# Kernel optimization log

Hardware: AMD Instinct MI355X
Metric: run time of the kernel (lower is better)

Reference implementation:

```python
import jax, jax.numpy as jnp
import numpy as np

EMBED_DIM = 256
H = 80
W = 80
N_HEADS = 8
N_POINTS = 4
B = 8


def sine_pe(C, h, w):
    # LoFTR-style PositionEncodingSine, returns [1, C, h, w]
    y_pos = jnp.cumsum(jnp.ones((h, w), jnp.float32), axis=0)[None]
    x_pos = jnp.cumsum(jnp.ones((h, w), jnp.float32), axis=1)[None]
    div = jnp.exp(jnp.arange(0, C // 2, 2, dtype=jnp.float32) * (-np.log(10000.0) / (C // 2)))[:, None, None]
    pe = jnp.zeros((C, h, w), jnp.float32)
    pe = pe.at[0::4].set(jnp.sin(x_pos * div))
    pe = pe.at[1::4].set(jnp.cos(x_pos * div))
    pe = pe.at[2::4].set(jnp.sin(y_pos * div))
    pe = pe.at[3::4].set(jnp.cos(y_pos * div))
    return pe[None]


def make_reference_points(h, w):
    # Faithful to the original (W-major flatten, (col, row) stacking)
    gr = np.linspace(0, 1, w)
    gc = np.linspace(0, 1, h)
    R, Cg = np.meshgrid(gr, gc, indexing='ij')  # (w, h)
    ref = np.stack((Cg, R), -1).reshape(-1, 2)  # [w*h, 2]
    return jnp.asarray(ref, jnp.float32)


def setup_inputs():
    key = jax.random.key(0)
    ks = jax.random.split(key, 8)
    C = EMBED_DIM
    s = 1.0 / np.sqrt(C)
    return {
        'query': jax.random.normal(ks[0], (B, C, H, W), jnp.float32),
        'value': jax.random.normal(ks[1], (B, C, H, W), jnp.float32),
        'W_value': jax.random.normal(ks[2], (C, C), jnp.float32) * s,
        'b_value': jnp.zeros((C,), jnp.float32),
        'W_off': jax.random.normal(ks[3], (C, N_HEADS * N_POINTS * 2), jnp.float32) * 0.01,
        'b_off': jax.random.normal(ks[4], (N_HEADS * N_POINTS * 2,), jnp.float32) * 0.5,
        'W_attn': jax.random.normal(ks[5], (C, N_HEADS * N_POINTS), jnp.float32) * s,
        'b_attn': jnp.zeros((N_HEADS * N_POINTS,), jnp.float32),
        'W_out': jax.random.normal(ks[6], (C, C), jnp.float32) * s,
        'b_out': jnp.zeros((C,), jnp.float32),
    }


def _deform_attn_core(q, v, ref, W_off, b_off, W_attn, b_attn):
    # q: [B, Nq, C] queries; v: [B, H*W, C] projected values; ref: [Nq, 2]
    Bq, Nq, C = q.shape
    hd = C // N_HEADS
    off = (q @ W_off + b_off).reshape(Bq, Nq, N_HEADS, N_POINTS, 2)
    aw = jax.nn.softmax((q @ W_attn + b_attn).reshape(Bq, Nq, N_HEADS, N_POINTS), axis=-1)
    norm = jnp.array([W, H], jnp.float32)  # offset normalizer (W, H), num_levels=1
    loc = ref[None, :, None, None, :] + off / norm  # [B, Nq, Hn, P, 2], normalized (x, y)
    loc = loc.transpose(0, 2, 1, 3, 4)  # [B, Hn, Nq, P, 2]
    # grid_sample(align_corners=False, padding_mode='zeros'): pixel = loc*size - 0.5
    x = loc[..., 0] * W - 0.5
    y = loc[..., 1] * H - 0.5
    x0f = jnp.floor(x); y0f = jnp.floor(y)
    wx = x - x0f; wy = y - y0f
    x0 = x0f.astype(jnp.int32); y0 = y0f.astype(jnp.int32)
    vh = v.reshape(Bq, H * W, N_HEADS, hd).transpose(0, 2, 1, 3)  # [B, Hn, HW, hd]

    def gather(ix, iy):
        valid = (ix >= 0) & (ix < W) & (iy >= 0) & (iy < H)
        idx = jnp.clip(iy, 0, H - 1) * W + jnp.clip(ix, 0, W - 1)  # [B, Hn, Nq, P]
        g = jnp.take_along_axis(vh, idx.reshape(Bq, N_HEADS, -1, 1), axis=2)
        return g.reshape(Bq, N_HEADS, Nq, N_POINTS, hd) * valid[..., None].astype(v.dtype)

    samp = (gather(x0, y0) * ((1 - wx) * (1 - wy))[..., None]
            + gather(x0 + 1, y0) * (wx * (1 - wy))[..., None]
            + gather(x0, y0 + 1) * ((1 - wx) * wy)[..., None]
            + gather(x0 + 1, y0 + 1) * (wx * wy)[..., None])  # [B, Hn, Nq, P, hd]
    out = jnp.einsum('bhqpd,bhqp->bqhd', samp, aw.transpose(0, 2, 1, 3))
    return out.reshape(Bq, Nq, C)


def reference(query, value, W_value, b_value, W_off, b_off, W_attn, b_attn, W_out, b_out):
    pe = sine_pe(EMBED_DIM, H, W)
    q = query + pe
    qf = q.reshape(B, EMBED_DIM, H * W).transpose(0, 2, 1)      # [B, Nq, C]
    vf = value.reshape(B, EMBED_DIM, H * W).transpose(0, 2, 1)  # [B, Nv, C]
    vproj = vf @ W_value + b_value
    ref = make_reference_points(H, W)
    attn = _deform_attn_core(qf, vproj, ref, W_off, b_off, W_attn, b_attn)
    attn = attn @ W_out + b_out
    attn = attn + qf  # mmcv MSDeformAttn residual (dropout identity at eval)
    out_img = attn.transpose(0, 2, 1).reshape(B, EMBED_DIM, H, W)
    # nn.Upsample(size=(H, W), bilinear) on an (H, W) map is identity (need_downsample=False)
    return (out_img + value, out_img)
```

## Files before the change

### kernel.cpp

```cpp
#include <hip/hip_runtime.h>
#include <hip/hip_bf16.h>
#include <stdint.h>

#define HH 80
#define WW 80
#define NQ 6400
#define CD 256
#define BB 8
#define OUT_HALF 13107200
#define PE_NEG 0.0719557841560639f

typedef __attribute__((ext_vector_type(4))) float f32x4;
typedef __bf16 bf16_t;
typedef __attribute__((ext_vector_type(8))) __bf16 bf16x8;
typedef __attribute__((ext_vector_type(4))) __bf16 bf16x4;
typedef _Float16 f16_t;
typedef __attribute__((ext_vector_type(8))) _Float16 f16x8;

using gp1_t = const __attribute__((address_space(1))) void*;
using lp3_t = __attribute__((address_space(3))) void*;

__device__ __forceinline__ void gload_lds16(const void* g, void* l) {
    __builtin_amdgcn_global_load_lds((gp1_t)g, (lp3_t)l, 16, 0, 0);
}

__global__ __launch_bounds__(256) void pe_kernel(float* __restrict__ pe) {
    int idx = blockIdx.x * 256 + threadIdx.x;
    if (idx >= CD * NQ) return;
    int c = idx / NQ, n = idx % NQ;
    int h = n / WW, w = n % WW;
    int k = c >> 2;
    float d = __expf((float)(2 * k) * -PE_NEG);
    float arg = ((c & 2) ? (float)(h + 1) : (float)(w + 1)) * d;
    float sv, cv;
    __sincosf(arg, &sv, &cv);
    pe[idx] = (c & 1) ? cv : sv;
}

__global__ __launch_bounds__(256) void wprep_kernel(const float* __restrict__ Wv,
                                                    const float* __restrict__ Woff,
                                                    const float* __restrict__ Wattn,
                                                    const float* __restrict__ Wout,
                                                    bf16_t* __restrict__ WvT,
                                                    bf16_t* __restrict__ WoaT,
                                                    bf16_t* __restrict__ WoT) {
    int idx = blockIdx.x * 256 + threadIdx.x;
    if (idx < 65536) {
        int cp = idx >> 8, c = idx & 255;
        WvT[idx] = (bf16_t)Wv[c * 256 + cp];
        WoT[idx] = (bf16_t)Wout[c * 256 + cp];
    }
    if (idx < 96 * 256) {
        int j = idx >> 8, c = idx & 255;
        WoaT[idx] = (bf16_t)(j < 64 ? Woff[c * 64 + j] : Wattn[c * 32 + (j - 64)]);
    }
}


__global__ __launch_bounds__(256, 3) void gemm_vproj(const float* __restrict__ V,
                                                     const bf16_t* __restrict__ Y,
                                                     const float* __restrict__ bias,
                                                     bf16_t* __restrict__ D) {
    __shared__ __align__(16) bf16_t lx[128 * 72];
    __shared__ __align__(16) bf16_t ly[128 * 64];
    int m0 = blockIdx.x * 128;
    int c0 = blockIdx.y * 128;
    int b = m0 / NQ, nloc = m0 % NQ;
    const float* src = V + (size_t)b * CD * NQ + nloc;
    int tid = threadIdx.x, wv = tid >> 6, ln = tid & 63;
    f32x4 acc[4][4] = {};
    int wr = (wv >> 1) * 64, wc = (wv & 1) * 64;
    int nl = tid & 31;
    for (int kt = 0; kt < 4; ++kt) {
#pragma unroll
        for (int q8 = 0; q8 < 4; ++q8) {
            int q = wv * 4 + q8;
            int row = q * 8 + (ln >> 3);
            int jj = (ln & 7) ^ (row & 7);
            gload_lds16((const char*)Y + ((size_t)(c0 + row)) * 512 + (size_t)kt * 128 + jj * 16,
                        (char*)ly + q * 1024);
        }
#pragma unroll
        for (int i = 0; i < 4; ++i) {
            int kp = (tid >> 5) + i * 8;
            int k = kp * 2;
            const float* s0 = src + (size_t)(kt * 64 + k) * NQ;
#pragma unroll
            for (int l = 0; l < 4; ++l) {
                int n = nl + 32 * l;
                float v0 = s0[n];
                float v1 = s0[NQ + n];
                union { bf16_t h[2]; uint32_t u; } pk;
                pk.h[0] = (bf16_t)v0; pk.h[1] = (bf16_t)v1;
                *(uint32_t*)((char*)lx + n * 144 + k * 2) = pk.u;
            }
        }
        __syncthreads();
#pragma unroll
        for (int ks = 0; ks < 2; ++ks) {
            bf16x8 xa[4], yb[4];
#pragma unroll
            for (int i = 0; i < 4; i++) {
                int m = wr + i * 16 + (ln & 15);
                xa[i] = *(const bf16x8*)((const char*)lx + m * 144 + ks * 64 + (ln >> 4) * 16);
                int n = wc + i * 16 + (ln & 15);
                int cn = (ks * 4 + (ln >> 4)) ^ (n & 7);
                yb[i] = *(const bf16x8*)((const char*)ly + n * 128 + cn * 16);
            }
#pragma unroll
            for (int i = 0; i < 4; i++)
#pragma unroll
                for (int j = 0; j < 4; j++)
                    acc[i][j] = __builtin_amdgcn_mfma_f32_16x16x32_bf16(xa[i], yb[j], acc[i][j], 0, 0, 0);
        }
        __syncthreads();
    }
#pragma unroll
    for (int i = 0; i < 4; i++)
#pragma unroll
        for (int j = 0; j < 4; j++) {
            int col = c0 + wc + j * 16 + (ln & 15);
            float bv = bias[col];
#pragma unroll
            for (int rg = 0; rg < 4; rg++) {
                int row = m0 + wr + i * 16 + (ln >> 4) * 4 + rg;
                D[(size_t)row * 256 + col] = (bf16_t)(acc[i][j][rg] + bv);
            }
        }
}

__global__ __launch_bounds__(256, 3) void gemm_oa(const float* __restrict__ Q,
                                                  const bf16_t* __restrict__ Y,
                                                  const float* __restrict__ boff,
                                                  const float* __restrict__ battn,
                                                  f16_t* __restrict__ D) {
    __shared__ __align__(16) bf16_t lx[128 * 72];
    __shared__ __align__(16) bf16_t ly[96 * 64];
    int m0 = blockIdx.x * 128;
    int b = m0 / NQ, nloc = m0 % NQ;
    const float* src = Q + (size_t)b * CD * NQ + nloc;
    int tid = threadIdx.x, wv = tid >> 6, ln = tid & 63;
    f32x4 acc[2][6] = {};
    int nl = tid & 31;
    for (int kt = 0; kt < 4; ++kt) {
#pragma unroll
        for (int q3 = 0; q3 < 3; ++q3) {
            int q = wv * 3 + q3;
            int row = q * 8 + (ln >> 3);
            int jj = (ln & 7) ^ (row & 7);
            gload_lds16((const char*)Y + ((size_t)row) * 512 + (size_t)kt * 128 + jj * 16,
                        (char*)ly + q * 1024);
        }
#pragma unroll
        for (int i = 0; i < 4; ++i) {
            int kp = (tid >> 5) + i * 8;
            int k = kp * 2;
            int c = kt * 64 + k;
            float d = __expf((float)(2 * (c >> 2)) * -PE_NEG);
            const float* s0 = src + (size_t)c * NQ;
#pragma unroll
            for (int l = 0; l < 4; ++l) {
                int n = nl + 32 * l;
                int p = nloc + n;
                int h = p / WW, w = p - h * WW;
                float pos = (c & 2) ? (float)(h + 1) : (float)(w + 1);
                float sv, cv;
                __sincosf(pos * d, &sv, &cv);
                float v0 = s0[n] + sv;
                float v1 = s0[NQ + n] + cv;
                union { bf16_t hh[2]; uint32_t u; } pk;
                pk.hh[0] = (bf16_t)v0; pk.hh[1] = (bf16_t)v1;
                *(uint32_t*)((char*)lx + n * 144 + k * 2) = pk.u;
            }
        }
        __syncthreads();
#pragma unroll
        for (int ks = 0; ks < 2; ++ks) {
            bf16x8 xa[2], yb[6];
#pragma unroll
            for (int i = 0; i < 2; i++) {
                int m = wv * 32 + i * 16 + (ln & 15);
                xa[i] = *(const bf16x8*)((const char*)lx + m * 144 + ks * 64 + (ln >> 4) * 16);
            }
#pragma unroll
            for (int j = 0; j < 6; j++) {
                int n = j * 16 + (ln & 15);
                int cn = (ks * 4 + (ln >> 4)) ^ (n & 7);
                yb[j] = *(const bf16x8*)((const char*)ly + n * 128 + cn * 16);
            }
#pragma unroll
            for (int i = 0; i < 2; i++)
#pragma unroll
                for (int j = 0; j < 6; j++)
                    acc[i][j] = __builtin_amdgcn_mfma_f32_16x16x32_bf16(xa[i], yb[j], acc[i][j], 0, 0, 0);
        }
        __syncthreads();
    }
#pragma unroll
    for (int i = 0; i < 2; i++)
#pragma unroll
        for (int j = 0; j < 6; j++) {
            int col = j * 16 + (ln & 15);
            float bv = col < 64 ? boff[col] : battn[col - 64];
#pragma unroll
            for (int rg = 0; rg < 4; rg++) {
                int row = m0 + wv * 32 + i * 16 + (ln >> 4) * 4 + rg;
                D[(size_t)row * 96 + col] = (f16_t)(acc[i][j][rg] + bv);
            }
        }
}

__global__ __launch_bounds__(256) void sample_kernel(const f16_t* __restrict__ oa,
                                                     const bf16_t* __restrict__ vp,
                                                     bf16_t* __restrict__ samp) {
    __shared__ float s[16][100];
    __shared__ float2 swo[16][8][17];
    int t = threadIdx.x;
    int bid = blockIdx.x;
    int b = bid & 7;
    int nq0 = (bid >> 3) * 16;
    size_t q0g = (size_t)b * NQ + nq0;
    if (t < 192) {
        int q = t / 12, e = (t % 12) * 8;
        f16x8 v = *(const f16x8*)(oa + (q0g + q) * 96 + e);
#pragma unroll
        for (int j = 0; j < 8; j++) s[q][e + j] = (float)v[j];
    }
    __syncthreads();
    if (t < 128) {
        int q = t >> 3, h = t & 7;
        int n = nq0 + q;
        const float* sq = s[q];
        float l0 = sq[64 + h * 4 + 0], l1 = sq[64 + h * 4 + 1];
        float l2 = sq[64 + h * 4 + 2], l3 = sq[64 + h * 4 + 3];
        float mx = fmaxf(fmaxf(l0, l1), fmaxf(l2, l3));
        float e0 = __expf(l0 - mx), e1 = __expf(l1 - mx), e2 = __expf(l2 - mx), e3 = __expf(l3 - mx);
        float inv = 1.f / (e0 + e1 + e2 + e3);
        float aw[4] = {e0 * inv, e1 * inv, e2 * inv, e3 * inv};
        float xb = (float)(n % WW) * (80.f / 79.f) - 0.5f;
        float yb = (float)(n / WW) * (80.f / 79.f) - 0.5f;
#pragma unroll
        for (int p = 0; p < 4; p++) {
            float x = xb + sq[h * 8 + p * 2];
            float y = yb + sq[h * 8 + p * 2 + 1];
            float x0f = floorf(x), y0f = floorf(y);
            float wx = x - x0f, wy = y - y0f;
            int ix = (int)x0f, iy = (int)y0f;
            bool vx0 = (unsigned)ix < (unsigned)WW, vx1 = (unsigned)(ix + 1) < (unsigned)WW;
            bool vy0 = (unsigned)iy < (unsigned)HH, vy1 = (unsigned)(iy + 1) < (unsigned)HH;
            int cx0 = min(max(ix, 0), WW - 1), cx1 = min(max(ix + 1, 0), WW - 1);
            int cy0 = min(max(iy, 0), HH - 1), cy1 = min(max(iy + 1, 0), HH - 1);
            float ap = aw[p];
            float w00 = (vx0 && vy0) ? ap * (1.f - wx) * (1.f - wy) : 0.f;
            float w10 = (vx1 && vy0) ? ap * wx * (1.f - wy) : 0.f;
            float w01 = (vx0 && vy1) ? ap * (1.f - wx) * wy : 0.f;
            float w11 = (vx1 && vy1) ? ap * wx * wy : 0.f;
            swo[q][h][p * 4 + 0] = make_float2(w00, __int_as_float(cy0 * WW + cx0));
            swo[q][h][p * 4 + 1] = make_float2(w10, __int_as_float(cy0 * WW + cx1));
            swo[q][h][p * 4 + 2] = make_float2(w01, __int_as_float(cy1 * WW + cx0));
            swo[q][h][p * 4 + 3] = make_float2(w11, __int_as_float(cy1 * WW + cx1));
        }
    }
    __syncthreads();
    int q = t >> 4, h = (t >> 1) & 7, sh = t & 1;
    const bf16_t* vb = vp + (size_t)b * NQ * CD + h * 32 + sh * 16;
    float acc[16];
#pragma unroll
    for (int j = 0; j < 16; j++) acc[j] = 0.f;
#pragma unroll
    for (int pc = 0; pc < 16; ++pc) {
        float2 wo = swo[q][h][pc];
        int off = __float_as_int(wo.y);
        const bf16x8* p8 = (const bf16x8*)(vb + (size_t)off * CD);
        bf16x8 v0 = p8[0], v1 = p8[1];
        float w = wo.x;
#pragma unroll
        for (int j = 0; j < 8; j++) acc[j] += (float)v0[j] * w;
#pragma unroll
        for (int j = 0; j < 8; j++) acc[8 + j] += (float)v1[j] * w;
    }
    bf16x8 o0, o1;
#pragma unroll
    for (int j = 0; j < 8; j++) { o0[j] = (bf16_t)acc[j]; o1[j] = (bf16_t)acc[8 + j]; }
    bf16x8* dst = (bf16x8*)(samp + (q0g + q) * CD + h * 32 + sh * 16);
    dst[0] = o0;
    dst[1] = o1;
}

__global__ __launch_bounds__(256, 4) void gemm_out(const bf16_t* __restrict__ X,
                                                   const bf16_t* __restrict__ Y,
                                                   const float* __restrict__ bout,
                                                   const float* __restrict__ query,
                                                   const float* __restrict__ value,
                                                   const float* __restrict__ pe,
                                                   float* __restrict__ out) {
    __shared__ __align__(16) char smem[32768];
    bf16_t* lx = (bf16_t*)smem;
    bf16_t* ly = (bf16_t*)(smem + 16384);
    float* tile = (float*)smem;
    int m0 = blockIdx.y * 128;
    int n0 = blockIdx.x * 128;
    int tid = threadIdx.x, wv = tid >> 6, ln = tid & 63;
    f32x4 acc[4][4] = {};
    int wr = (wv >> 1) * 64, wc = (wv & 1) * 64;
    for (int kt = 0; kt < 4; ++kt) {
#pragma unroll
        for (int q8 = 0; q8 < 4; ++q8) {
            int q = wv * 4 + q8;
            int row = q * 8 + (ln >> 3);
            int jj = (ln & 7) ^ (row & 7);
            gload_lds16((const char*)X + ((size_t)(m0 + row)) * 512 + (size_t)kt * 128 + jj * 16,
                        (char*)lx + q * 1024);
            gload_lds16((const char*)Y + ((size_t)(n0 + row)) * 512 + (size_t)kt * 128 + jj * 16,
                        (char*)ly + q * 1024);
        }
        __syncthreads();
#pragma unroll
        for (int ks = 0; ks < 2; ++ks) {
            bf16x8 xa[4], yb[4];
#pragma unroll
            for (int i = 0; i < 4; i++) {
                int m = wr + i * 16 + (ln & 15);
                int ch = (ks * 4 + (ln >> 4)) ^ (m & 7);
                xa[i] = *(const bf16x8*)((const char*)lx + m * 128 + ch * 16);
                int n = wc + i * 16 + (ln & 15);
                int cn = (ks * 4 + (ln >> 4)) ^ (n & 7);
                yb[i] = *(const bf16x8*)((const char*)ly + n * 128 + cn * 16);
            }
#pragma unroll
            for (int i = 0; i < 4; i++)
#pragma unroll
                for (int j = 0; j < 4; j++)
                    acc[i][j] = __builtin_amdgcn_mfma_f32_16x16x32_bf16(xa[i], yb[j], acc[i][j], 0, 0, 0);
        }
        __syncthreads();
    }
    int b = n0 / NQ;
    int nb = n0 - b * NQ;
    const float* qp = query + (size_t)b * CD * NQ;
    const float* vp = value + (size_t)b * CD * NQ;
    float* o0 = out + (size_t)b * CD * NQ;
    float* o1 = out + OUT_HALF + (size_t)b * CD * NQ;
#pragma unroll
    for (int pass = 0; pass < 2; ++pass) {
        if ((wv >> 1) == pass) {
#pragma unroll
            for (int i = 0; i < 4; i++)
#pragma unroll
                for (int j = 0; j < 4; j++) {
                    int c = wc + j * 16 + (ln & 15);
#pragma unroll
                    for (int rg = 0; rg < 4; rg++) {
                        int r = i * 16 + (ln >> 4) * 4 + rg;
                        tile[r * 128 + c] = acc[i][j][rg] + bout[m0 + pass * 64 + r];
                    }
                }
        }
        __syncthreads();
        int g4 = (ln & 31) * 4;
        int rb = wv * 16 + (ln >> 5);
#pragma unroll
        for (int jj = 0; jj < 8; ++jj) {
            int r = rb + jj * 2;
            int crow = m0 + pass * 64 + r;
            size_t off = (size_t)crow * NQ + nb + g4;
            f32x4 tv = *(const f32x4*)&tile[r * 128 + g4];
            f32x4 qv = *(const f32x4*)(qp + off);
            f32x4 pv = *(const f32x4*)(pe + off);
            f32x4 vv = *(const f32x4*)(vp + off);
            f32x4 o1v = tv + qv + pv;
            *(f32x4*)(o1 + off) = o1v;
            *(f32x4*)(o0 + off) = o1v + vv;
        }
        __syncthreads();
    }
}

extern "C" void kernel_launch(void* const* d_in, const int* in_sizes, int n_in,
                              void* d_out, int out_size, void* d_ws, size_t ws_size,
                              hipStream_t stream) {
    const float* query   = (const float*)d_in[0];
    const float* value   = (const float*)d_in[1];
    const float* W_value = (const float*)d_in[2];
    const float* b_value = (const float*)d_in[3];
    const float* W_off   = (const float*)d_in[4];
    const float* b_off   = (const float*)d_in[5];
    const float* W_attn  = (const float*)d_in[6];
    const float* b_attn  = (const float*)d_in[7];
    const float* W_out   = (const float*)d_in[8];
    const float* b_out   = (const float*)d_in[9];
    float* out = (float*)d_out;
    char* ws = (char*)d_ws;

    float*  pe    = (float*)(ws + 0);
    bf16_t* WvT   = (bf16_t*)(ws + 6553600);
    bf16_t* WoT   = (bf16_t*)(ws + 6684672);
    bf16_t* WoaT  = (bf16_t*)(ws + 6815744);
    bf16_t* vprojB= (bf16_t*)(ws + 6864896);
    f16_t*  oaH   = (f16_t*)(ws + 33079296);
    bf16_t* samp  = (bf16_t*)(ws + 42909696);

    pe_kernel<<<(CD * NQ + 255) / 256, 256, 0, stream>>>(pe);
    wprep_kernel<<<256, 256, 0, stream>>>(W_value, W_off, W_attn, W_out, WvT, WoaT, WoT);
    gemm_vproj<<<dim3(400, 2), 256, 0, stream>>>(value, WvT, b_value, vprojB);
    gemm_oa<<<dim3(400), 256, 0, stream>>>(query, WoaT, b_off, b_attn, oaH);
    sample_kernel<<<3200, 256, 0, stream>>>(oaH, vprojB, samp);
    gemm_out<<<dim3(400, 2), 256, 0, stream>>>(WoT, samp, b_out, query, value, pe, out);
}
```

Before: 121.6 us.

## Fuse offset/attention GEMM with sampling and compute positional encoding inline

Merges the offset/attention-logit GEMM with the bilinear sampling kernel, keeping the per-query offsets and logits in shared memory instead of writing them to global memory and reading them back. Removes the separate positional-encoding kernel and recomputes the sine/cosine encoding inside the output GEMM epilogue. This cuts two launches and the global round trips for the PE buffer and the offset buffer. In exchange, the fused kernel runs fewer, heavier blocks with lower occupancy, and the epilogue does extra transcendental math.

```diff
diff --git a/kernel.cpp b/kernel.cpp
--- a/kernel.cpp
+++ b/kernel.cpp
@@ -13,28 +13,13 @@
 typedef __attribute__((ext_vector_type(4))) float f32x4;
 typedef __bf16 bf16_t;
 typedef __attribute__((ext_vector_type(8))) __bf16 bf16x8;
-typedef __attribute__((ext_vector_type(4))) __bf16 bf16x4;
 typedef _Float16 f16_t;
-typedef __attribute__((ext_vector_type(8))) _Float16 f16x8;
 
 using gp1_t = const __attribute__((address_space(1))) void*;
 using lp3_t = __attribute__((address_space(3))) void*;
 
 __device__ __forceinline__ void gload_lds16(const void* g, void* l) {
     __builtin_amdgcn_global_load_lds((gp1_t)g, (lp3_t)l, 16, 0, 0);
-}
-
-__global__ __launch_bounds__(256) void pe_kernel(float* __restrict__ pe) {
-    int idx = blockIdx.x * 256 + threadIdx.x;
-    if (idx >= CD * NQ) return;
-    int c = idx / NQ, n = idx % NQ;
-    int h = n / WW, w = n % WW;
-    int k = c >> 2;
-    float d = __expf((float)(2 * k) * -PE_NEG);
-    float arg = ((c & 2) ? (float)(h + 1) : (float)(w + 1)) * d;
-    float sv, cv;
-    __sincosf(arg, &sv, &cv);
-    pe[idx] = (c & 1) ? cv : sv;
 }
 
 __global__ __launch_bounds__(256) void wprep_kernel(const float* __restrict__ Wv,
@@ -55,7 +40,6 @@
         WoaT[idx] = (bf16_t)(j < 64 ? Woff[c * 64 + j] : Wattn[c * 32 + (j - 64)]);
     }
 }
-
 
 __global__ __launch_bounds__(256, 3) void gemm_vproj(const float* __restrict__ V,
                                                      const bf16_t* __restrict__ Y,
@@ -129,15 +113,19 @@
         }
 }
 
-__global__ __launch_bounds__(256, 3) void gemm_oa(const float* __restrict__ Q,
-                                                  const bf16_t* __restrict__ Y,
-                                                  const float* __restrict__ boff,
-                                                  const float* __restrict__ battn,
-                                                  f16_t* __restrict__ D) {
+__global__ __launch_bounds__(256, 2) void oa_sample(const float* __restrict__ Q,
+                                                    const bf16_t* __restrict__ Y,
+                                                    const float* __restrict__ boff,
+                                                    const float* __restrict__ battn,
+                                                    const bf16_t* __restrict__ vp,
+                                                    bf16_t* __restrict__ samp) {
     __shared__ __align__(16) bf16_t lx[128 * 72];
     __shared__ __align__(16) bf16_t ly[96 * 64];
-    int m0 = blockIdx.x * 128;
-    int b = m0 / NQ, nloc = m0 % NQ;
+    __shared__ f16_t oaT[128][100];
+    int bid = blockIdx.x;
+    int b = bid & 7;
+    int nloc = (bid >> 3) * 128;
+    int m0 = b * NQ + nloc;
     const float* src = Q + (size_t)b * CD * NQ + nloc;
     int tid = threadIdx.x, wv = tid >> 6, ln = tid & 63;
     f32x4 acc[2][6] = {};
@@ -204,45 +192,32 @@
             float bv = col < 64 ? boff[col] : battn[col - 64];
 #pragma unroll
             for (int rg = 0; rg < 4; rg++) {
-                int row = m0 + wv * 32 + i * 16 + (ln >> 4) * 4 + rg;
-                D[(size_t)row * 96 + col] = (f16_t)(acc[i][j][rg] + bv);
-            }
-        }
-}
-
-__global__ __launch_bounds__(256) void sample_kernel(const f16_t* __restrict__ oa,
-                                                     const bf16_t* __restrict__ vp,
-                                                     bf16_t* __restrict__ samp) {
-    __shared__ float s[16][100];
-    __shared__ float2 swo[16][8][17];
-    int t = threadIdx.x;
-    int bid = blockIdx.x;
-    int b = bid & 7;
-    int nq0 = (bid >> 3) * 16;
-    size_t q0g = (size_t)b * NQ + nq0;
-    if (t < 192) {
-        int q = t / 12, e = (t % 12) * 8;
-        f16x8 v = *(const f16x8*)(oa + (q0g + q) * 96 + e);
-#pragma unroll
-        for (int j = 0; j < 8; j++) s[q][e + j] = (float)v[j];
-    }
+                int rloc = wv * 32 + i * 16 + (ln >> 4) * 4 + rg;
+                oaT[rloc][col] = (f16_t)(acc[i][j][rg] + bv);
+            }
+        }
     __syncthreads();
-    if (t < 128) {
-        int q = t >> 3, h = t & 7;
-        int n = nq0 + q;
-        const float* sq = s[q];
-        float l0 = sq[64 + h * 4 + 0], l1 = sq[64 + h * 4 + 1];
-        float l2 = sq[64 + h * 4 + 2], l3 = sq[64 + h * 4 + 3];
+    int h = (tid >> 1) & 7, sh = tid & 1;
+    const bf16_t* vb = vp + (size_t)b * NQ * CD + h * 32 + sh * 16;
+#pragma unroll
+    for (int rnd = 0; rnd < 8; ++rnd) {
+        int q = rnd * 16 + (tid >> 4);
+        int n = nloc + q;
+        const f16_t* sq = oaT[q];
+        float l0 = (float)sq[64 + h * 4 + 0], l1 = (float)sq[64 + h * 4 + 1];
+        float l2 = (float)sq[64 + h * 4 + 2], l3 = (float)sq[64 + h * 4 + 3];
         float mx = fmaxf(fmaxf(l0, l1), fmaxf(l2, l3));
         float e0 = __expf(l0 - mx), e1 = __expf(l1 - mx), e2 = __expf(l2 - mx), e3 = __expf(l3 - mx);
         float inv = 1.f / (e0 + e1 + e2 + e3);
         float aw[4] = {e0 * inv, e1 * inv, e2 * inv, e3 * inv};
         float xb = (float)(n % WW) * (80.f / 79.f) - 0.5f;
         float yb = (float)(n / WW) * (80.f / 79.f) - 0.5f;
+        float wgt[16];
+        int idx[16];
 #pragma unroll
         for (int p = 0; p < 4; p++) {
-            float x = xb + sq[h * 8 + p * 2];
-            float y = yb + sq[h * 8 + p * 2 + 1];
+            float x = xb + (float)sq[h * 8 + p * 2];
+            float y = yb + (float)sq[h * 8 + p * 2 + 1];
             float x0f = floorf(x), y0f = floorf(y);
             float wx = x - x0f, wy = y - y0f;
             int ix = (int)x0f, iy = (int)y0f;
@@ -251,40 +226,35 @@
             int cx0 = min(max(ix, 0), WW - 1), cx1 = min(max(ix + 1, 0), WW - 1);
             int cy0 = min(max(iy, 0), HH - 1), cy1 = min(max(iy + 1, 0), HH - 1);
             float ap = aw[p];
-            float w00 = (vx0 && vy0) ? ap * (1.f - wx) * (1.f - wy) : 0.f;
-            float w10 = (vx1 && vy0) ? ap * wx * (1.f - wy) : 0.f;
-            float w01 = (vx0 && vy1) ? ap * (1.f - wx) * wy : 0.f;
-            float w11 = (vx1 && vy1) ? ap * wx * wy : 0.f;
-            swo[q][h][p * 4 + 0] = make_float2(w00, __int_as_float(cy0 * WW + cx0));
-            swo[q][h][p * 4 + 1] = make_float2(w10, __int_as_float(cy0 * WW + cx1));
-            swo[q][h][p * 4 + 2] = make_float2(w01, __int_as_float(cy1 * WW + cx0));
-            swo[q][h][p * 4 + 3] = make_float2(w11, __int_as_float(cy1 * WW + cx1));
-        }
-    }
-    __syncthreads();
-    int q = t >> 4, h = (t >> 1) & 7, sh = t & 1;
-    const bf16_t* vb = vp + (size_t)b * NQ * CD + h * 32 + sh * 16;
-    float acc[16];
-#pragma unroll
-    for (int j = 0; j < 16; j++) acc[j] = 0.f;
-#pragma unroll
-    for (int pc = 0; pc < 16; ++pc) {
-        float2 wo = swo[q][h][pc];
-        int off = __float_as_int(wo.y);
-        const bf16x8* p8 = (const bf16x8*)(vb + (size_t)off * CD);
-        bf16x8 v0 = p8[0], v1 = p8[1];
-        float w = wo.x;
-#pragma unroll
-        for (int j = 0; j < 8; j++) acc[j] += (float)v0[j] * w;
-#pragma unroll
-        for (int j = 0; j < 8; j++) acc[8 + j] += (float)v1[j] * w;
-    }
-    bf16x8 o0, o1;
-#pragma unroll
-    for (int j = 0; j < 8; j++) { o0[j] = (bf16_t)acc[j]; o1[j] = (bf16_t)acc[8 + j]; }
-    bf16x8* dst = (bf16x8*)(samp + (q0g + q) * CD + h * 32 + sh * 16);
-    dst[0] = o0;
-    dst[1] = o1;
+            wgt[p * 4 + 0] = (vx0 && vy0) ? ap * (1.f - wx) * (1.f - wy) : 0.f;
+            wgt[p * 4 + 1] = (vx1 && vy0) ? ap * wx * (1.f - wy) : 0.f;
+            wgt[p * 4 + 2] = (vx0 && vy1) ? ap * (1.f - wx) * wy : 0.f;
+            wgt[p * 4 + 3] = (vx1 && vy1) ? ap * wx * wy : 0.f;
+            idx[p * 4 + 0] = cy0 * WW + cx0;
+            idx[p * 4 + 1] = cy0 * WW + cx1;
+            idx[p * 4 + 2] = cy1 * WW + cx0;
+            idx[p * 4 + 3] = cy1 * WW + cx1;
+        }
+        float fac[16];
+#pragma unroll
+        for (int j = 0; j < 16; j++) fac[j] = 0.f;
+#pragma unroll
+        for (int pc = 0; pc < 16; ++pc) {
+            const bf16x8* p8 = (const bf16x8*)(vb + (size_t)idx[pc] * CD);
+            bf16x8 v0 = p8[0], v1 = p8[1];
+            float w = wgt[pc];
+#pragma unroll
+            for (int j = 0; j < 8; j++) fac[j] += (float)v0[j] * w;
+#pragma unroll
+            for (int j = 0; j < 8; j++) fac[8 + j] += (float)v1[j] * w;
+        }
+        bf16x8 o0, o1;
+#pragma unroll
+        for (int j = 0; j < 8; j++) { o0[j] = (bf16_t)fac[j]; o1[j] = (bf16_t)fac[8 + j]; }
+        bf16x8* dst = (bf16x8*)(samp + (size_t)(m0 + q) * CD + h * 32 + sh * 16);
+        dst[0] = o0;
+        dst[1] = o1;
+    }
 }
 
 __global__ __launch_bounds__(256, 4) void gemm_out(const bf16_t* __restrict__ X,
@@ -292,7 +262,6 @@
                                                    const float* __restrict__ bout,
                                                    const float* __restrict__ query,
                                                    const float* __restrict__ value,
-                                                   const float* __restrict__ pe,
                                                    float* __restrict__ out) {
     __shared__ __align__(16) char smem[32768];
     bf16_t* lx = (bf16_t*)smem;
@@ -366,8 +335,19 @@
             size_t off = (size_t)crow * NQ + nb + g4;
             f32x4 tv = *(const f32x4*)&tile[r * 128 + g4];
             f32x4 qv = *(const f32x4*)(qp + off);
-            f32x4 pv = *(const f32x4*)(pe + off);
             f32x4 vv = *(const f32x4*)(vp + off);
+            float d = __expf((float)(2 * (crow >> 2)) * -PE_NEG);
+            bool useY = (crow & 2) != 0, odd = (crow & 1) != 0;
+            f32x4 pv;
+#pragma unroll
+            for (int e = 0; e < 4; ++e) {
+                int n = nb + g4 + e;
+                int hh = n / WW, ww = n - hh * WW;
+                float pos = useY ? (float)(hh + 1) : (float)(ww + 1);
+                float sv, cv;
+                __sincosf(pos * d, &sv, &cv);
+                pv[e] = odd ? cv : sv;
+            }
             f32x4 o1v = tv + qv + pv;
             *(f32x4*)(o1 + off) = o1v;
             *(f32x4*)(o0 + off) = o1v + vv;
@@ -392,18 +372,14 @@
     float* out = (float*)d_out;
     char* ws = (char*)d_ws;
 
-    float*  pe    = (float*)(ws + 0);
-    bf16_t* WvT   = (bf16_t*)(ws + 6553600);
-    bf16_t* WoT   = (bf16_t*)(ws + 6684672);
-    bf16_t* WoaT  = (bf16_t*)(ws + 6815744);
-    bf16_t* vprojB= (bf16_t*)(ws + 6864896);
-    f16_t*  oaH   = (f16_t*)(ws + 33079296);
-    bf16_t* samp  = (bf16_t*)(ws + 42909696);
-
-    pe_kernel<<<(CD * NQ + 255) / 256, 256, 0, stream>>>(pe);
+    bf16_t* WvT   = (bf16_t*)(ws + 0);
+    bf16_t* WoT   = (bf16_t*)(ws + 131072);
+    bf16_t* WoaT  = (bf16_t*)(ws + 262144);
+    bf16_t* vprojB= (bf16_t*)(ws + 311296);
+    bf16_t* samp  = (bf16_t*)(ws + 26525696);
+
     wprep_kernel<<<256, 256, 0, stream>>>(W_value, W_off, W_attn, W_out, WvT, WoaT, WoT);
     gemm_vproj<<<dim3(400, 2), 256, 0, stream>>>(value, WvT, b_value, vprojB);
-    gemm_oa<<<dim3(400), 256, 0, stream>>>(query, WoaT, b_off, b_attn, oaH);
-    sample_kernel<<<3200, 256, 0, stream>>>(oaH, vprojB, samp);
-    gemm_out<<<dim3(400, 2), 256, 0, stream>>>(WoT, samp, b_out, query, value, pe, out);
-}
+    oa_sample<<<400, 256, 0, stream>>>(query, WoaT, b_off, b_attn, vprojB, samp);
+    gemm_out<<<dim3(400, 2), 256, 0, stream>>>(WoT, samp, b_out, query, value, out);
+}
```

After: 110.1 us. 9.4% less time.
